# Performance work log

Measured on AMD Instinct MI355X. Metric: run time of the kernel, lower is better.

## Reference

```python
import jax, jax.numpy as jnp
import numpy as np

N_NODES = 40000


def setup_inputs() -> dict:
    key = jax.random.key(0)
    k_h, k_w, k_b, k_s, k_d = jax.random.split(key, 5)
    in_feats, out_feats, n_edges = 128, 128, 640000
    h = jax.random.normal(k_h, (N_NODES, in_feats), dtype=jnp.float32)
    # nn.Linear(in_feats, out_feats): weight [out, in], bias [out]
    W = jax.random.normal(k_w, (out_feats, in_feats), dtype=jnp.float32) * (1.0 / np.sqrt(in_feats))
    b = jax.random.normal(k_b, (out_feats,), dtype=jnp.float32) * 0.01
    src = jax.random.randint(k_s, (n_edges,), 0, N_NODES, dtype=jnp.int32)
    dst = jax.random.randint(k_d, (n_edges,), 0, N_NODES, dtype=jnp.int32)
    return {"h": h, "W": W, "b": b, "src": src, "dst": dst}


def reference(h, W, b, src, dst):
    # update_all(copy_u('h','m'), sum('m','h_N')):
    # gather messages from source nodes, segment-sum into destination nodes.
    msgs = h[src]                                              # [E, in_feats] irregular gather
    agg = jax.ops.segment_sum(msgs, dst, num_segments=N_NODES)  # [N, in_feats] scatter-add
    # Source module applies the linear to h (agg is computed but unused there);
    # we return agg as a second output so the SpMM is observable.
    out = h @ W.T + b                                          # [N, out_feats]
    return out, agg
```

## Files before the change

kernel.cpp:

```cpp
#include <hip/hip_runtime.h>

#define FEAT 128
#define CAP  64

typedef short bf16x8 __attribute__((ext_vector_type(8)));
typedef float f32x4  __attribute__((ext_vector_type(4)));

__device__ __forceinline__ unsigned pack_bf16x2(float x, float y) {
    unsigned ux = __float_as_uint(x);
    ux = (ux + 0x7fffu + ((ux >> 16) & 1u)) >> 16;
    unsigned uy = __float_as_uint(y);
    uy = (uy + 0x7fffu + ((uy >> 16) & 1u)) & 0xffff0000u;
    return uy | ux;
}

__device__ __forceinline__ bf16x8 pack8(float4 a, float4 b) {
    uint4 u = make_uint4(pack_bf16x2(a.x, a.y), pack_bf16x2(a.z, a.w),
                         pack_bf16x2(b.x, b.y), pack_bf16x2(b.z, b.w));
    return __builtin_bit_cast(bf16x8, u);
}

__device__ __forceinline__ f32x4 unpack2(uint2 v) {
    return (f32x4){__uint_as_float(v.x << 16), __uint_as_float(v.x & 0xffff0000u),
                   __uint_as_float(v.y << 16), __uint_as_float(v.y & 0xffff0000u)};
}

__global__ __launch_bounds__(256) void fused_gemm_convert_kernel(
    const float* __restrict__ h, const float* __restrict__ W,
    const float* __restrict__ b, float* __restrict__ out,
    unsigned* __restrict__ hb, int* __restrict__ counts,
    int nrows, int gemm_blocks, int nh_units, int nzero_units)
{
    const int bid = blockIdx.x;
    const int tid = threadIdx.x;

    if (bid >= gemm_blocks) {
        int gid = (bid - gemm_blocks) * 256 + tid;
        if (gid < nzero_units) ((uint4*)counts)[gid] = make_uint4(0u, 0u, 0u, 0u);
        if (gid < nh_units) {
            float4 v = ((const float4*)h)[gid];
            ((uint2*)hb)[gid] = make_uint2(pack_bf16x2(v.x, v.y), pack_bf16x2(v.z, v.w));
        }
        return;
    }

    const int wid  = bid * 4 + (tid >> 6);
    const int lane = tid & 63;
    const int m    = lane & 15, quad = lane >> 4;
    const int r0g  = wid * 32;
    if (r0g >= nrows) return;

    const float4* __restrict__ h4 = (const float4*)h;
    const float4* __restrict__ W4 = (const float4*)W;

    bf16x8 af[2][4];
#pragma unroll
    for (int mt = 0; mt < 2; ++mt) {
        int gr = r0g + mt * 16 + m;
#pragma unroll
        for (int ks = 0; ks < 4; ++ks) {
            float4 a0 = h4[(size_t)gr * 32 + ks * 8 + quad * 2];
            float4 a1 = h4[(size_t)gr * 32 + ks * 8 + quad * 2 + 1];
            af[mt][ks] = pack8(a0, a1);
        }
    }

    f32x4 acc[2][8];
#pragma unroll
    for (int mt = 0; mt < 2; ++mt)
#pragma unroll
        for (int n = 0; n < 8; ++n) acc[mt][n] = (f32x4){0.f, 0.f, 0.f, 0.f};

#pragma unroll
    for (int n = 0; n < 8; ++n) {
        int c = n * 16 + m;
#pragma unroll
        for (int ks = 0; ks < 4; ++ks) {
            float4 b0 = W4[(size_t)c * 32 + ks * 8 + quad * 2];
            float4 b1 = W4[(size_t)c * 32 + ks * 8 + quad * 2 + 1];
            bf16x8 bf = pack8(b0, b1);
#pragma unroll
            for (int mt = 0; mt < 2; ++mt)
                acc[mt][n] = __builtin_amdgcn_mfma_f32_16x16x32_bf16(
                    af[mt][ks], bf, acc[mt][n], 0, 0, 0);
        }
    }

#pragma unroll
    for (int n = 0; n < 8; ++n) {
        float bias = b[n * 16 + m];
#pragma unroll
        for (int mt = 0; mt < 2; ++mt)
#pragma unroll
            for (int r = 0; r < 4; ++r) {
                int gr = r0g + mt * 16 + quad * 4 + r;
                if (gr < nrows) out[(size_t)gr * FEAT + n * 16 + m] = acc[mt][n][r] + bias;
            }
    }
}

__global__ __launch_bounds__(256) void fill_bucket_kernel(
    const int* __restrict__ src, const int* __restrict__ dst,
    int* __restrict__ counts, int* __restrict__ bucket, int E)
{
    int e = blockIdx.x * 256 + threadIdx.x;
    if (e >= E) return;
    int d = dst[e];
    int pos = atomicAdd(&counts[d], 1);
    if (pos < CAP) bucket[d * CAP + pos] = src[e];
}

__global__ __launch_bounds__(256) void gather_bucket_kernel(
    const unsigned* __restrict__ hb, const int* __restrict__ counts,
    const int* __restrict__ bucket, float* __restrict__ agg, int N)
{
    int gid  = blockIdx.x * 256 + threadIdx.x;
    int node = gid >> 6;
    int lane = gid & 63;
    if (node >= N) return;

    int deg = counts[node];
    deg = (deg > CAP) ? CAP : deg;
    int eid = bucket[node * CAP + lane];

    const uint2* __restrict__ hb2 = (const uint2*)hb;
    const int l5 = lane & 31, half = lane >> 5;

    f32x4 a0 = (f32x4){0.f, 0.f, 0.f, 0.f};
    f32x4 a1 = (f32x4){0.f, 0.f, 0.f, 0.f};

    int t = 0;
    for (; t + 4 <= deg; t += 4) {
        int s0 = __shfl(eid, t + half);
        int s1 = __shfl(eid, t + 2 + half);
        uint2 v0 = hb2[(size_t)s0 * 32 + l5];
        uint2 v1 = hb2[(size_t)s1 * 32 + l5];
        a0 += unpack2(v0);
        a1 += unpack2(v1);
    }
    if (t + 2 <= deg) {
        int s = __shfl(eid, t + half);
        uint2 v = hb2[(size_t)s * 32 + l5];
        a0 += unpack2(v);
        t += 2;
    }
    if (t < deg) {
        int s = __shfl(eid, t);
        uint2 v = hb2[(size_t)s * 32 + l5];
        if (half == 0) a1 += unpack2(v);
    }
    a0 += a1;

    a0[0] += __shfl_down(a0[0], 32);
    a0[1] += __shfl_down(a0[1], 32);
    a0[2] += __shfl_down(a0[2], 32);
    a0[3] += __shfl_down(a0[3], 32);

    if (half == 0) {
        float4 o = make_float4(a0[0], a0[1], a0[2], a0[3]);
        ((float4*)agg)[(size_t)node * 32 + l5] = o;
    }
}

__global__ __launch_bounds__(256, 2) void gemm_f32_kernel(
    const float* __restrict__ h, const float* __restrict__ W,
    const float* __restrict__ b, float* __restrict__ out, int nrows)
{
    __shared__ float4 wsh[128 * 8];
    __shared__ float4 hsh[64 * 8];
    const int tid = threadIdx.x;
    const int tx  = tid & 31;
    const int ty  = tid >> 5;
    const int r0  = blockIdx.x * 64;
    const float4* __restrict__ W4 = (const float4*)W;
    const float4* __restrict__ h4 = (const float4*)h;
    float acc[8][4];
#pragma unroll
    for (int i = 0; i < 8; ++i)
#pragma unroll
        for (int j = 0; j < 4; ++j) acc[i][j] = 0.f;
    for (int p = 0; p < 4; ++p) {
        if (p) __syncthreads();
#pragma unroll
        for (int l = 0; l < 4; ++l) {
            int flat = l * 256 + tid;
            int c = flat >> 3, kc = flat & 7;
            wsh[c * 8 + (kc ^ ((c >> 2) & 7))] = W4[c * 32 + p * 8 + kc];
        }
#pragma unroll
        for (int l = 0; l < 2; ++l) {
            int flat = l * 256 + tid;
            int r = flat >> 3, kc = flat & 7;
            int gr = r0 + r;
            float4 v = make_float4(0.f, 0.f, 0.f, 0.f);
            if (gr < nrows) v = h4[(size_t)gr * 32 + p * 8 + kc];
            hsh[r * 8 + (kc ^ ((r >> 2) & 7))] = v;
        }
        __syncthreads();
#pragma unroll
        for (int kc = 0; kc < 8; ++kc) {
            float4 wv[4], hv[8];
#pragma unroll
            for (int j = 0; j < 4; ++j) wv[j] = wsh[(4 * tx + j) * 8 + (kc ^ (tx & 7))];
#pragma unroll
            for (int i = 0; i < 8; ++i) {
                int r = 8 * ty + i;
                hv[i] = hsh[r * 8 + (kc ^ ((r >> 2) & 7))];
            }
#pragma unroll
            for (int i = 0; i < 8; ++i)
#pragma unroll
                for (int j = 0; j < 4; ++j) {
                    acc[i][j] += hv[i].x * wv[j].x;
                    acc[i][j] += hv[i].y * wv[j].y;
                    acc[i][j] += hv[i].z * wv[j].z;
                    acc[i][j] += hv[i].w * wv[j].w;
                }
        }
    }
    const float4 bj = ((const float4*)b)[tx];
    float4* out4 = (float4*)out;
#pragma unroll
    for (int i = 0; i < 8; ++i) {
        int gr = r0 + 8 * ty + i;
        if (gr < nrows) {
            float4 o;
            o.x = acc[i][0] + bj.x; o.y = acc[i][1] + bj.y;
            o.z = acc[i][2] + bj.z; o.w = acc[i][3] + bj.w;
            out4[(size_t)gr * 32 + tx] = o;
        }
    }
}

__global__ __launch_bounds__(256) void scatter_add_kernel(
    const float* __restrict__ h, const int* __restrict__ src,
    const int* __restrict__ dst, float* __restrict__ agg, int E)
{
    int gid  = blockIdx.x * 256 + threadIdx.x;
    int e    = gid >> 6;
    int lane = gid & 63;
    if (e >= E) return;
    int s = src[e];
    int d = dst[e];
    const float2* hp = (const float2*)(h + (size_t)s * FEAT);
    float2 v = hp[lane];
    float* ap = agg + (size_t)d * FEAT + 2 * lane;
    unsafeAtomicAdd(ap,     v.x);
    unsafeAtomicAdd(ap + 1, v.y);
}

extern "C" void kernel_launch(void* const* d_in, const int* in_sizes, int n_in,
                              void* d_out, int out_size, void* d_ws, size_t ws_size,
                              hipStream_t stream) {
    const float* h   = (const float*)d_in[0];
    const float* W   = (const float*)d_in[1];
    const float* b   = (const float*)d_in[2];
    const int*   src = (const int*)d_in[3];
    const int*   dst = (const int*)d_in[4];

    const int n = in_sizes[0] / FEAT;
    const int E = in_sizes[3];

    float* out = (float*)d_out;
    float* agg = out + (size_t)n * FEAT;

    size_t hb_bytes     = (size_t)n * FEAT * 2;
    size_t bucket_bytes = (size_t)n * CAP * 4;
    size_t counts_bytes = (size_t)n * 4;
    size_t need = hb_bytes + bucket_bytes + counts_bytes;

    if (ws_size >= need) {
        unsigned* hb     = (unsigned*)d_ws;
        int*      bucket = (int*)((char*)d_ws + hb_bytes);
        int*      counts = (int*)((char*)d_ws + hb_bytes + bucket_bytes);

        int gemm_blocks  = (n + 127) / 128;
        int nh_units     = n * FEAT / 4;
        int nzero_units  = (n + 3) / 4;
        int conv_blocks  = (nh_units + 255) / 256;

        fused_gemm_convert_kernel<<<dim3(gemm_blocks + conv_blocks), dim3(256), 0, stream>>>(
            h, W, b, out, hb, counts, n, gemm_blocks, nh_units, nzero_units);

        fill_bucket_kernel<<<dim3((E + 255) / 256), dim3(256), 0, stream>>>(
            src, dst, counts, bucket, E);

        gather_bucket_kernel<<<dim3((int)(((long long)n * 64 + 255) / 256)), dim3(256), 0, stream>>>(
            hb, counts, bucket, agg, n);
    } else {
        gemm_f32_kernel<<<dim3((n + 63) / 64), dim3(256), 0, stream>>>(h, W, b, out, n);
        hipMemsetAsync(agg, 0, (size_t)n * FEAT * sizeof(float), stream);
        int nblocks = (int)(((long long)E * 64 + 255) / 256);
        scatter_add_kernel<<<dim3(nblocks), dim3(256), 0, stream>>>(h, src, dst, agg, E);
    }
}
```

Baseline: 161.5 us.

## Fuse bucket fill into GEMM kernel and reuse GEMM bf16 fragments for hb

The GEMM warps now write the bf16 copy of h straight from the A fragments they already packed, so the separate conversion pass that re-read h is gone. The edge-bucketing work runs as extra blocks of the same launch, and counts are zeroed with a memset beforehand, which turns three kernels into a memset plus two. The gather now loads 16-byte bf16 rows and handles 4 edges per wavefront step instead of 2, and only reads bucket entries below the degree. In exchange the fill blocks compete with GEMM blocks inside one launch, and the bf16 layout of hb has to match the fragment ordering exactly.

```diff
diff --git a/kernel.cpp b/kernel.cpp
--- a/kernel.cpp
+++ b/kernel.cpp
@@ -20,26 +20,27 @@
     return __builtin_bit_cast(bf16x8, u);
 }
 
-__device__ __forceinline__ f32x4 unpack2(uint2 v) {
-    return (f32x4){__uint_as_float(v.x << 16), __uint_as_float(v.x & 0xffff0000u),
-                   __uint_as_float(v.y << 16), __uint_as_float(v.y & 0xffff0000u)};
-}
-
-__global__ __launch_bounds__(256) void fused_gemm_convert_kernel(
+__device__ __forceinline__ f32x4 unpack2(unsigned x, unsigned y) {
+    return (f32x4){__uint_as_float(x << 16), __uint_as_float(x & 0xffff0000u),
+                   __uint_as_float(y << 16), __uint_as_float(y & 0xffff0000u)};
+}
+
+__global__ __launch_bounds__(256) void fused_kernel(
     const float* __restrict__ h, const float* __restrict__ W,
-    const float* __restrict__ b, float* __restrict__ out,
-    unsigned* __restrict__ hb, int* __restrict__ counts,
-    int nrows, int gemm_blocks, int nh_units, int nzero_units)
+    const float* __restrict__ b, const int* __restrict__ src,
+    const int* __restrict__ dst, float* __restrict__ out,
+    uint4* __restrict__ hb4, int* __restrict__ counts, int* __restrict__ bucket,
+    int nrows, int gemm_blocks, int E)
 {
     const int bid = blockIdx.x;
     const int tid = threadIdx.x;
 
     if (bid >= gemm_blocks) {
-        int gid = (bid - gemm_blocks) * 256 + tid;
-        if (gid < nzero_units) ((uint4*)counts)[gid] = make_uint4(0u, 0u, 0u, 0u);
-        if (gid < nh_units) {
-            float4 v = ((const float4*)h)[gid];
-            ((uint2*)hb)[gid] = make_uint2(pack_bf16x2(v.x, v.y), pack_bf16x2(v.z, v.w));
+        int e = (bid - gemm_blocks) * 256 + tid;
+        if (e < E) {
+            int d = dst[e];
+            int pos = atomicAdd(&counts[d], 1);
+            if (pos < CAP) bucket[d * CAP + pos] = src[e];
         }
         return;
     }
@@ -65,6 +66,16 @@
         }
     }
 
+#pragma unroll
+    for (int mt = 0; mt < 2; ++mt) {
+        int gr = r0g + mt * 16 + m;
+        if (gr < nrows) {
+#pragma unroll
+            for (int ks = 0; ks < 4; ++ks)
+                hb4[(size_t)gr * 16 + ks * 4 + quad] = __builtin_bit_cast(uint4, af[mt][ks]);
+        }
+    }
+
     f32x4 acc[2][8];
 #pragma unroll
     for (int mt = 0; mt < 2; ++mt)
@@ -99,19 +110,8 @@
     }
 }
 
-__global__ __launch_bounds__(256) void fill_bucket_kernel(
-    const int* __restrict__ src, const int* __restrict__ dst,
-    int* __restrict__ counts, int* __restrict__ bucket, int E)
-{
-    int e = blockIdx.x * 256 + threadIdx.x;
-    if (e >= E) return;
-    int d = dst[e];
-    int pos = atomicAdd(&counts[d], 1);
-    if (pos < CAP) bucket[d * CAP + pos] = src[e];
-}
-
 __global__ __launch_bounds__(256) void gather_bucket_kernel(
-    const unsigned* __restrict__ hb, const int* __restrict__ counts,
+    const uint4* __restrict__ hb4, const int* __restrict__ counts,
     const int* __restrict__ bucket, float* __restrict__ agg, int N)
 {
     int gid  = blockIdx.x * 256 + threadIdx.x;
@@ -121,44 +121,52 @@
 
     int deg = counts[node];
     deg = (deg > CAP) ? CAP : deg;
-    int eid = bucket[node * CAP + lane];
-
-    const uint2* __restrict__ hb2 = (const uint2*)hb;
-    const int l5 = lane & 31, half = lane >> 5;
-
-    f32x4 a0 = (f32x4){0.f, 0.f, 0.f, 0.f};
-    f32x4 a1 = (f32x4){0.f, 0.f, 0.f, 0.f};
+    int eid = (lane < deg) ? bucket[node * CAP + lane] : 0;
+
+    const int q = lane >> 4, ql = lane & 15;
+
+    f32x4 al0 = {0.f,0.f,0.f,0.f}, ah0 = {0.f,0.f,0.f,0.f};
+    f32x4 al1 = {0.f,0.f,0.f,0.f}, ah1 = {0.f,0.f,0.f,0.f};
 
     int t = 0;
-    for (; t + 4 <= deg; t += 4) {
-        int s0 = __shfl(eid, t + half);
-        int s1 = __shfl(eid, t + 2 + half);
-        uint2 v0 = hb2[(size_t)s0 * 32 + l5];
-        uint2 v1 = hb2[(size_t)s1 * 32 + l5];
-        a0 += unpack2(v0);
-        a1 += unpack2(v1);
-    }
-    if (t + 2 <= deg) {
-        int s = __shfl(eid, t + half);
-        uint2 v = hb2[(size_t)s * 32 + l5];
-        a0 += unpack2(v);
-        t += 2;
-    }
-    if (t < deg) {
-        int s = __shfl(eid, t);
-        uint2 v = hb2[(size_t)s * 32 + l5];
-        if (half == 0) a1 += unpack2(v);
-    }
-    a0 += a1;
-
-    a0[0] += __shfl_down(a0[0], 32);
-    a0[1] += __shfl_down(a0[1], 32);
-    a0[2] += __shfl_down(a0[2], 32);
-    a0[3] += __shfl_down(a0[3], 32);
-
-    if (half == 0) {
-        float4 o = make_float4(a0[0], a0[1], a0[2], a0[3]);
-        ((float4*)agg)[(size_t)node * 32 + l5] = o;
+    for (; t + 8 <= deg; t += 8) {
+        int s0 = __shfl(eid, t + q);
+        int s1 = __shfl(eid, t + 4 + q);
+        uint4 v0 = hb4[(size_t)s0 * 16 + ql];
+        uint4 v1 = hb4[(size_t)s1 * 16 + ql];
+        al0 += unpack2(v0.x, v0.y);
+        ah0 += unpack2(v0.z, v0.w);
+        al1 += unpack2(v1.x, v1.y);
+        ah1 += unpack2(v1.z, v1.w);
+    }
+    {
+        int i0 = t + q, i1 = t + 4 + q;
+        int s0 = __shfl(eid, i0 & 63);
+        int s1 = __shfl(eid, i1 & 63);
+        if (i0 < deg) {
+            uint4 v = hb4[(size_t)s0 * 16 + ql];
+            al0 += unpack2(v.x, v.y);
+            ah0 += unpack2(v.z, v.w);
+        }
+        if (i1 < deg) {
+            uint4 v = hb4[(size_t)s1 * 16 + ql];
+            al1 += unpack2(v.x, v.y);
+            ah1 += unpack2(v.z, v.w);
+        }
+    }
+    al0 += al1; ah0 += ah1;
+
+#pragma unroll
+    for (int j = 0; j < 4; ++j) {
+        al0[j] += __shfl_down(al0[j], 32);
+        ah0[j] += __shfl_down(ah0[j], 32);
+        al0[j] += __shfl_down(al0[j], 16);
+        ah0[j] += __shfl_down(ah0[j], 16);
+    }
+
+    if (q == 0) {
+        ((float4*)agg)[(size_t)node * 32 + ql * 2]     = make_float4(al0[0], al0[1], al0[2], al0[3]);
+        ((float4*)agg)[(size_t)node * 32 + ql * 2 + 1] = make_float4(ah0[0], ah0[1], ah0[2], ah0[3]);
     }
 }
 
@@ -270,20 +278,16 @@
     size_t need = hb_bytes + bucket_bytes + counts_bytes;
 
     if (ws_size >= need) {
-        unsigned* hb     = (unsigned*)d_ws;
-        int*      bucket = (int*)((char*)d_ws + hb_bytes);
-        int*      counts = (int*)((char*)d_ws + hb_bytes + bucket_bytes);
-
-        int gemm_blocks  = (n + 127) / 128;
-        int nh_units     = n * FEAT / 4;
-        int nzero_units  = (n + 3) / 4;
-        int conv_blocks  = (nh_units + 255) / 256;
-
-        fused_gemm_convert_kernel<<<dim3(gemm_blocks + conv_blocks), dim3(256), 0, stream>>>(
-            h, W, b, out, hb, counts, n, gemm_blocks, nh_units, nzero_units);
-
-        fill_bucket_kernel<<<dim3((E + 255) / 256), dim3(256), 0, stream>>>(
-            src, dst, counts, bucket, E);
+        uint4* hb     = (uint4*)d_ws;
+        int*   bucket = (int*)((char*)d_ws + hb_bytes);
+        int*   counts = (int*)((char*)d_ws + hb_bytes + bucket_bytes);
+
+        hipMemsetAsync(counts, 0, counts_bytes, stream);
+
+        int gemm_blocks = (n + 127) / 128;
+        int fill_blocks = (E + 255) / 256;
+        fused_kernel<<<dim3(gemm_blocks + fill_blocks), dim3(256), 0, stream>>>(
+            h, W, b, src, dst, out, hb, counts, bucket, n, gemm_blocks, E);
 
         gather_bucket_kernel<<<dim3((int)(((long long)n * 64 + 255) / 256)), dim3(256), 0, stream>>>(
             hb, counts, bucket, agg, n);
```

Measured after the change: 147.5 us. -8.6%, faster.
